# Optimization experiments

Hardware: AMD Instinct MI355X
Metric: run time of the kernel (lower is better)

Reference implementation:

```python
import jax, jax.numpy as jnp
import numpy as np

B, S, D, H = 2, 2048, 2048, 32
DH = D // H
NEG = -1e9


def setup_inputs() -> dict:
    key = jax.random.key(0)
    ks = jax.random.split(key, 10)
    sc = 0.02
    hidden_state = jax.random.normal(ks[0], (B, S, D), dtype=jnp.float32)
    # additive causal mask, broadcastable to [B,H,S,S]
    causal = jnp.tril(jnp.ones((S, S), dtype=bool))
    mask = jnp.where(causal, 0.0, NEG).astype(jnp.float32)[None, None]
    return {
        "hidden_state": hidden_state,
        "mask": mask,
        "q_w": jax.random.normal(ks[1], (D, D), jnp.float32) * sc,
        "q_b": jnp.zeros((D,), jnp.float32),
        "k_w": jax.random.normal(ks[2], (D, D), jnp.float32) * sc,
        "k_b": jnp.zeros((D,), jnp.float32),
        "v_w": jax.random.normal(ks[3], (D, D), jnp.float32) * sc,
        "v_b": jnp.zeros((D,), jnp.float32),
        "o_w": jax.random.normal(ks[4], (D, D), jnp.float32) * sc,
        "o_b": jnp.zeros((D,), jnp.float32),
    }


def reference(hidden_state, mask, q_w, q_b, k_w, k_b, v_w, v_b, o_w, o_b):
    scale = DH ** -0.5
    # projections (torch Linear: x @ W^T + b)
    q = (hidden_state @ q_w.T + q_b).reshape(B, S, H, DH).transpose(0, 2, 1, 3) * scale
    k = (hidden_state @ k_w.T + k_b).reshape(B, S, H, DH).transpose(0, 2, 1, 3)
    v = (hidden_state @ v_w.T + v_b).reshape(B, S, H, DH).transpose(0, 2, 1, 3)
    qk = jnp.einsum('bhqd,bhkd->bhqk', q, k) + mask
    attn = jax.nn.softmax(qk, axis=-1)
    o = jnp.einsum('bhqk,bhkd->bhqd', attn, v)
    o = o.transpose(0, 2, 1, 3).reshape(B, S, D)
    return o @ o_w.T + o_b
```

## Files before the change

### kernel.cpp

```cpp
#include <hip/hip_runtime.h>
#include <stdint.h>

#define Hh   32
#define Ss   2048
#define Dd   2048
#define DHd  64
#define Mtok 4096
#define MiB  (1u << 20)
#define NTK  32

typedef unsigned short u16;
typedef u16   u16x4  __attribute__((ext_vector_type(4)));
typedef u16   u16x8  __attribute__((ext_vector_type(8)));
typedef short bf16x8 __attribute__((ext_vector_type(8)));
typedef float f32x4  __attribute__((ext_vector_type(4)));

__device__ __forceinline__ u16 f2bf(float f) {
    union { float f; uint32_t u; } v; v.f = f;
    uint32_t r = v.u + 0x7fffu + ((v.u >> 16) & 1u);
    return (u16)(r >> 16);
}
__device__ __forceinline__ uint32_t cvtpk_bf16(float lo, float hi) {
    uint32_t r;
    asm volatile("v_cvt_pk_bf16_f32 %0, %1, %2" : "=v"(r) : "v"(lo), "v"(hi));
    return r;
}
__device__ __forceinline__ void gld_lds16(const void* g, void* l) {
    __builtin_amdgcn_global_load_lds(
        (const __attribute__((address_space(1))) uint32_t*)g,
        (__attribute__((address_space(3))) uint32_t*)l,
        16, 0, 0);
}
#define SB() __builtin_amdgcn_sched_barrier(0)

__global__ void cvt_all(const float* __restrict__ x,  const float* __restrict__ qw,
                        const float* __restrict__ kw, const float* __restrict__ vw,
                        const float* __restrict__ ow,
                        u16* __restrict__ Xb, u16* __restrict__ Wcat, u16* __restrict__ Wob)
{
    const size_t nX = 1u << 23, nW = 1u << 22;
    size_t i = ((size_t)blockIdx.x * 256 + threadIdx.x) * 8;
    const float* src; u16* dst; size_t off;
    if (i < nX) { src = x; dst = Xb; off = i; }
    else {
        size_t j = i - nX;
        int seg = (int)(j >> 22);
        off = j & (nW - 1);
        src = (seg == 0) ? qw : (seg == 1) ? kw : (seg == 2) ? vw : ow;
        dst = (seg == 3) ? Wob : Wcat + (size_t)seg * nW;
    }
    f32x4 a = *(const f32x4*)(src + off);
    f32x4 b = *(const f32x4*)(src + off + 4);
    u16x8 o;
    o[0] = f2bf(a[0]); o[1] = f2bf(a[1]); o[2] = f2bf(a[2]); o[3] = f2bf(a[3]);
    o[4] = f2bf(b[0]); o[5] = f2bf(b[1]); o[6] = f2bf(b[2]); o[7] = f2bf(b[3]);
    *(u16x8*)(dst + off) = o;
}


__device__ __forceinline__ void stage_unitA(const u16* __restrict__ src, u16* dst, int wid, int lane)
{
    const int P = wid * 64 + lane;
    const int rp = P >> 3, c4p = P & 7, c4 = c4p ^ (rp & 7);
    const int r = rp * 2 + (c4 >> 2), c = (c4 & 3) * 8;
    gld_lds16(src + (size_t)r * Dd + c, dst + wid * 512);
}
__device__ __forceinline__ void stage_unitB(const u16* __restrict__ src, u16* dst, int wid, int lane)
{
#pragma unroll
    for (int j = 0; j < 2; ++j) {
        const int P = j * 512 + wid * 64 + lane;
        const int rp = P >> 3, c4p = P & 7, c4 = c4p ^ (rp & 7);
        const int r = rp * 2 + (c4 >> 2), c = (c4 & 3) * 8;
        gld_lds16(src + (size_t)r * Dd + c, dst + j * 4096 + wid * 512);
    }
}
__device__ __forceinline__ bf16x8 frag_read(const u16* unit, int r, int lg)
{
    const int rp = r >> 1;
    const int c4 = ((r & 1) << 2) | lg;
    const int c4p = c4 ^ (rp & 7);
    return *(const bf16x8*)(unit + rp * 64 + c4p * 8);
}

__device__ __forceinline__ void gemm2_core(const u16* __restrict__ Ab, const u16* __restrict__ Wb,
                                           u16* L, f32x4 acc[4][4],
                                           int wid, int lane, int l15, int lg, int wm, int wn)
{
    u16* const L0 = L;
    u16* const L1 = L + 24576;
    stage_unitA(Ab + 0,  L0 + 0,     wid, lane);
    stage_unitB(Wb + 0,  L0 + 8192,  wid, lane);
    stage_unitA(Ab + 32, L0 + 4096,  wid, lane);
    stage_unitB(Wb + 32, L0 + 16384, wid, lane);
    stage_unitA(Ab + 64, L1 + 0,     wid, lane);
    stage_unitB(Wb + 64, L1 + 8192,  wid, lane);
    asm volatile("s_waitcnt vmcnt(6)" ::: "memory");
    SB(); __builtin_amdgcn_s_barrier(); SB();

    const int aro = wm * 64 + l15;
    const int bro = wn * 64 + l15;
#pragma unroll 2
    for (int t = 0; t < NTK; ++t) {
        u16* const Lc = (t & 1) ? L1 : L0;
        u16* const Ln = (t & 1) ? L0 : L1;
#pragma unroll
        for (int ph = 0; ph < 2; ++ph) {
            const u16* Au = Lc + ph * 4096;
            const u16* Bu = Lc + 8192 + ph * 8192;
            bf16x8 bfr[4], a[4];
#pragma unroll
            for (int ni = 0; ni < 4; ++ni) bfr[ni] = frag_read(Bu, bro + ni * 16, lg);
#pragma unroll
            for (int mi = 0; mi < 4; ++mi) a[mi] = frag_read(Au, aro + mi * 16, lg);
            if (ph == 0) {
                if (t + 1 < NTK) {
                    stage_unitA(Ab + (t + 1) * 64 + 32, Ln + 4096,  wid, lane);
                    stage_unitB(Wb + (t + 1) * 64 + 32, Ln + 16384, wid, lane);
                }
            } else {
                if (t + 2 < NTK) {
                    stage_unitA(Ab + (t + 2) * 64, Lc + 0,    wid, lane);
                    stage_unitB(Wb + (t + 2) * 64, Lc + 8192, wid, lane);
                }
            }
            asm volatile("s_waitcnt lgkmcnt(0)" ::: "memory");
            SB();
            __builtin_amdgcn_s_setprio(1);
#pragma unroll
            for (int mi = 0; mi < 4; ++mi)
#pragma unroll
                for (int ni = 0; ni < 4; ++ni)
                    acc[mi][ni] = __builtin_amdgcn_mfma_f32_16x16x32_bf16(a[mi], bfr[ni], acc[mi][ni], 0, 0, 0);
            __builtin_amdgcn_s_setprio(0);
            const bool deep = (ph == 0) ? (t + 1 < NTK) : (t + 2 < NTK);
            if (deep) { asm volatile("s_waitcnt vmcnt(6)" ::: "memory"); }
            else      { asm volatile("s_waitcnt vmcnt(0)" ::: "memory"); }
            SB(); __builtin_amdgcn_s_barrier(); SB();
        }
    }
}

__global__ __launch_bounds__(512) void gemm_qkv8(
    const u16* __restrict__ X, const u16* __restrict__ Wcat,
    const float* __restrict__ Bq, const float* __restrict__ Bk, const float* __restrict__ Bv,
    u16* __restrict__ Qo, u16* __restrict__ Ko, u16* __restrict__ Vo)
{
    __shared__ __align__(16) u16 L[2 * 24576];
    const int tid = threadIdx.x, wid = tid >> 6, lane = tid & 63;
    const int l15 = lane & 15, lg = lane >> 4;
    const int wm = wid >> 2, wn = wid & 3;
    const int m0 = blockIdx.x * 128, n0 = blockIdx.y * 256;

    f32x4 acc[4][4] = {};
    gemm2_core(X + (size_t)m0 * Dd, Wcat + (size_t)n0 * Dd, L, acc, wid, lane, l15, lg, wm, wn);

#pragma unroll
    for (int ni = 0; ni < 4; ++ni) {
        const int n = n0 + wn * 64 + ni * 16 + l15;
        const int z = n >> 11, nn = n & 2047;
        const float bv = (z == 0 ? Bq : z == 1 ? Bk : Bv)[nn];
        const float sc = (z == 0) ? 0.125f : 1.0f;
        u16* Out = (z == 0 ? Qo : z == 1 ? Ko : Vo);
        const int h = nn >> 6, dh = nn & 63;
#pragma unroll
        for (int mi = 0; mi < 4; ++mi)
#pragma unroll
            for (int r = 0; r < 4; ++r) {
                const int m = m0 + wm * 64 + mi * 16 + lg * 4 + r;
                const int b = m >> 11, s = m & 2047;
                Out[(((size_t)b * Hh + h) * Ss + s) * DHd + dh] = f2bf((acc[mi][ni][r] + bv) * sc);
            }
    }
}

__global__ __launch_bounds__(512) void gemm_oproj8(
    const u16* __restrict__ A, const u16* __restrict__ W,
    const float* __restrict__ Bi, float* __restrict__ Out)
{
    __shared__ __align__(16) u16 L[2 * 24576];
    const int tid = threadIdx.x, wid = tid >> 6, lane = tid & 63;
    const int l15 = lane & 15, lg = lane >> 4;
    const int wm = wid >> 2, wn = wid & 3;
    const int m0 = blockIdx.x * 128, n0 = blockIdx.y * 256;

    f32x4 acc[4][4] = {};
    gemm2_core(A + (size_t)m0 * Dd, W + (size_t)n0 * Dd, L, acc, wid, lane, l15, lg, wm, wn);

#pragma unroll
    for (int ni = 0; ni < 4; ++ni) {
        const int n = n0 + wn * 64 + ni * 16 + l15;
        const float bv = Bi[n];
#pragma unroll
        for (int mi = 0; mi < 4; ++mi)
#pragma unroll
            for (int r = 0; r < 4; ++r) {
                const int m = m0 + wm * 64 + mi * 16 + lg * 4 + r;
                Out[(size_t)m * Dd + n] = acc[mi][ni][r] + bv;
            }
    }
}

__global__ void transpose_v(const u16* __restrict__ Vsrc, u16* __restrict__ Vdst)
{
    __shared__ __align__(16) u16 t[64 * 68];
    const int bh = blockIdx.y, s0 = blockIdx.x * 64;
    const int tid = threadIdx.x;
    {
        const int r = tid >> 2, cq = (tid & 3) * 16;
        const u16* src = Vsrc + ((size_t)bh * Ss + s0 + r) * DHd;
#pragma unroll
        for (int j = 0; j < 4; ++j) {
            u16x4 v = *(const u16x4*)(src + cq + j * 4);
            *(u16x4*)&t[r * 68 + cq + j * 4] = v;
        }
    }
    __syncthreads();
    {
        const int d = tid >> 2, sq = (tid & 3) * 16;
        u16* dst = Vdst + ((size_t)bh * DHd + d) * Ss + s0;
#pragma unroll
        for (int j = 0; j < 4; ++j) {
            u16x4 v;
            v.x = t[(sq + j * 4 + 0) * 68 + d];
            v.y = t[(sq + j * 4 + 1) * 68 + d];
            v.z = t[(sq + j * 4 + 2) * 68 + d];
            v.w = t[(sq + j * 4 + 3) * 68 + d];
            *(u16x4*)(dst + sq + j * 4) = v;
        }
    }
}

__device__ __forceinline__ void stage_kv(const u16* __restrict__ Kg, const u16* __restrict__ Vg,
                                         u16* Kl, u16* Vl, int kv0, int tid)
{
    const int u    = tid;
    const int row  = u >> 3;
    const int csrc = ((u & 7) ^ (row & 7)) * 8;
    const int base = (u & ~63) * 8;
    gld_lds16(Kg + (size_t)(kv0 + row) * DHd + csrc, Kl + base);
    gld_lds16(Vg + (size_t)row * Ss + kv0 + csrc, Vl + base);
}

__device__ __forceinline__ void attn_tile(
    const u16* __restrict__ Kc, const u16* __restrict__ Vc, int kv0,
    int q0, int qrow, int l15, int lg, int psw,
    const bf16x8* __restrict__ bq, f32x4* __restrict__ o,
    float& m_r, float& l_r, char* __restrict__ prow)
{
    if (kv0 > q0 + 15) return;
    f32x4 s[4] = {};
    __builtin_amdgcn_s_setprio(1);
#pragma unroll
    for (int nb = 0; nb < 4; ++nb) {
        const int krow = nb * 16 + l15;
        const char* rb = (const char*)(Kc + krow * 64);
        const int sw = (krow & 7) << 4;
#pragma unroll
        for (int kf = 0; kf < 2; ++kf) {
            bf16x8 ak = *(const bf16x8*)(rb + ((kf * 64 + lg * 16) ^ sw));
            s[nb] = __builtin_amdgcn_mfma_f32_16x16x32_bf16(ak, bq[kf], s[nb], 0, 0, 0);
        }
    }
    __builtin_amdgcn_s_setprio(0);
    if (kv0 + 63 > q0) {
#pragma unroll
        for (int nb = 0; nb < 4; ++nb)
#pragma unroll
            for (int r = 0; r < 4; ++r)
                if (kv0 + nb * 16 + lg * 4 + r > qrow) s[nb][r] = -3e38f;
    }
    float pm = -3e38f;
#pragma unroll
    for (int nb = 0; nb < 4; ++nb)
#pragma unroll
        for (int r = 0; r < 4; ++r) pm = fmaxf(pm, s[nb][r]);
    pm = fmaxf(pm, __shfl_xor(pm, 16, 64));
    pm = fmaxf(pm, __shfl_xor(pm, 32, 64));
    const bool full = !__all(pm - m_r <= 8.0f);
    float mn = m_r, al = 1.0f;
    if (full) {
        mn = fmaxf(m_r, pm);
        al = __expf(m_r - mn);
#pragma unroll
        for (int nb = 0; nb < 4; ++nb)
#pragma unroll
            for (int r = 0; r < 4; ++r) o[nb][r] *= al;
    }
    float rs = 0.f;
    float p[4][4];
#pragma unroll
    for (int nb = 0; nb < 4; ++nb)
#pragma unroll
        for (int r = 0; r < 4; ++r) { p[nb][r] = __expf(s[nb][r] - mn); rs += p[nb][r]; }
    rs += __shfl_xor(rs, 16, 64);
    rs += __shfl_xor(rs, 32, 64);
    l_r = l_r * al + rs;
    m_r = mn;
#pragma unroll
    for (int nb = 0; nb < 4; ++nb) {
        const uint32_t w0 = cvtpk_bf16(p[nb][0], p[nb][1]);
        const uint32_t w1 = cvtpk_bf16(p[nb][2], p[nb][3]);
        const int c0 = (nb * 32 + lg * 8) ^ psw;
        *(uint32_t*)(prow + c0)     = w0;
        *(uint32_t*)(prow + c0 + 4) = w1;
    }
    bf16x8 pa[2];
#pragma unroll
    for (int ks = 0; ks < 2; ++ks)
        pa[ks] = *(const bf16x8*)(prow + ((ks * 64 + lg * 16) ^ psw));
    __builtin_amdgcn_s_setprio(1);
#pragma unroll
    for (int nb = 0; nb < 4; ++nb) {
        const int vrow = nb * 16 + l15;
        const char* rb = (const char*)(Vc + vrow * 64);
        const int sw = (vrow & 7) << 4;
#pragma unroll
        for (int ks = 0; ks < 2; ++ks) {
            bf16x8 bv = *(const bf16x8*)(rb + ((ks * 64 + lg * 16) ^ sw));
            o[nb] = __builtin_amdgcn_mfma_f32_16x16x32_bf16(bv, pa[ks], o[nb], 0, 0, 0);
        }
    }
    __builtin_amdgcn_s_setprio(0);
}

__global__ __launch_bounds__(512) void attn(
    const u16* __restrict__ Qb, const u16* __restrict__ Kb,
    const u16* __restrict__ Vt, u16* __restrict__ Ob)
{
    __shared__ __align__(16) u16 Kl[2][4096];
    __shared__ __align__(16) u16 Vl[2][4096];
    __shared__ __align__(16) u16 PlA[8][1024];
    __shared__ __align__(16) u16 PlB[8][1024];
    const int bh = blockIdx.y;
    const int b = bh >> 5, h = bh & 31;
    const int tid = threadIdx.x;
    const int wid = tid >> 6, lane = tid & 63;
    const int l15 = lane & 15, lg = lane >> 4;
    const int bxA = blockIdx.x, bxB = 15 - bxA;
    const int q0A = bxA * 128 + wid * 16, q0B = bxB * 128 + wid * 16;
    const int qrowA = q0A + l15, qrowB = q0B + l15;
    char* prowA = (char*)PlA[wid] + l15 * 128;
    char* prowB = (char*)PlB[wid] + l15 * 128;
    const int psw = (l15 & 7) << 4;

    const u16* Kp = Kb + (size_t)bh * Ss * DHd;
    const u16* Vp = Vt + (size_t)bh * DHd * Ss;

    bf16x8 bqA[2], bqB[2];
    {
        const u16* QpA = Qb + ((size_t)bh * Ss + q0A) * DHd;
        const u16* QpB = Qb + ((size_t)bh * Ss + q0B) * DHd;
#pragma unroll
        for (int kf = 0; kf < 2; ++kf) {
            bqA[kf] = *(const bf16x8*)(QpA + (size_t)l15 * DHd + kf * 32 + lg * 8);
            bqB[kf] = *(const bf16x8*)(QpB + (size_t)l15 * DHd + kf * 32 + lg * 8);
        }
    }
    asm volatile("s_waitcnt vmcnt(0)" ::: "memory");

    f32x4 oA[4] = {}, oB[4] = {};
    float mA = -3e38f, lA = 0.f, mB = -3e38f, lB = 0.f;
    const int nt = 2 * (bxB + 1);

    stage_kv(Kp, Vp, Kl[0], Vl[0], 0, tid);
    for (int t = 0; t < nt; ++t) {
        if (t + 1 < nt) {
            stage_kv(Kp, Vp, Kl[(t + 1) & 1], Vl[(t + 1) & 1], (t + 1) * 64, tid);
            asm volatile("s_waitcnt vmcnt(2)" ::: "memory");
        } else {
            asm volatile("s_waitcnt vmcnt(0)" ::: "memory");
        }
        SB(); __builtin_amdgcn_s_barrier(); SB();
        const int kv0 = t * 64;
        attn_tile(Kl[t & 1], Vl[t & 1], kv0, q0A, qrowA, l15, lg, psw, bqA, oA, mA, lA, prowA);
        attn_tile(Kl[t & 1], Vl[t & 1], kv0, q0B, qrowB, l15, lg, psw, bqB, oB, mB, lB, prowB);
        SB(); __builtin_amdgcn_s_barrier(); SB();
    }

    {
        const float inv = 1.0f / lA;
        u16* orow = Ob + ((size_t)b * Ss + qrowA) * Dd + h * DHd;
#pragma unroll
        for (int nb = 0; nb < 4; ++nb) {
            u16x4 pk;
#pragma unroll
            for (int r = 0; r < 4; ++r) pk[r] = f2bf(oA[nb][r] * inv);
            *(u16x4*)(orow + nb * 16 + lg * 4) = pk;
        }
    }
    {
        const float inv = 1.0f / lB;
        u16* orow = Ob + ((size_t)b * Ss + qrowB) * Dd + h * DHd;
#pragma unroll
        for (int nb = 0; nb < 4; ++nb) {
            u16x4 pk;
#pragma unroll
            for (int r = 0; r < 4; ++r) pk[r] = f2bf(oB[nb][r] * inv);
            *(u16x4*)(orow + nb * 16 + lg * 4) = pk;
        }
    }
}

extern "C" void kernel_launch(void* const* d_in, const int* in_sizes, int n_in,
                              void* d_out, int out_size, void* d_ws, size_t ws_size,
                              hipStream_t stream)
{
    (void)in_sizes; (void)n_in; (void)out_size; (void)ws_size;
    const float* x  = (const float*)d_in[0];
    const float* qw = (const float*)d_in[2];
    const float* qb = (const float*)d_in[3];
    const float* kw = (const float*)d_in[4];
    const float* kb = (const float*)d_in[5];
    const float* vw = (const float*)d_in[6];
    const float* vb = (const float*)d_in[7];
    const float* ow = (const float*)d_in[8];
    const float* obias = (const float*)d_in[9];

    uint8_t* ws = (uint8_t*)d_ws;
    u16* Xb  = (u16*)(ws);
    u16* Wcat= (u16*)(ws + 16 * MiB);
    u16* Wob = (u16*)(ws + 40 * MiB);
    u16* Qb  = (u16*)(ws + 48 * MiB);
    u16* Kb  = (u16*)(ws + 64 * MiB);
    u16* Vb  = (u16*)(ws + 80 * MiB);
    u16* Vt  = Xb;
    u16* Ob  = Vb;

    cvt_all<<<12288, 256, 0, stream>>>(x, qw, kw, vw, ow, Xb, Wcat, Wob);

    gemm_qkv8<<<dim3(Mtok / 128, 6144 / 256), dim3(512), 0, stream>>>(
        Xb, Wcat, qb, kb, vb, Qb, Kb, Vb);
    transpose_v<<<dim3(Ss / 64, 64), dim3(256), 0, stream>>>(Vb, Vt);
    attn<<<dim3(8, 64), dim3(512), 0, stream>>>(Qb, Kb, Vt, Ob);
    gemm_oproj8<<<dim3(Mtok / 128, Dd / 256), dim3(512), 0, stream>>>(
        Ob, Wob, obias, (float*)d_out);
}
```

Before: 239.2 us.

## Load GEMM A fragments directly from global, shrink LDS, swizzle block order

The GEMM core no longer stages the activation (A) tile through LDS. Each wave reads its A fragments straight from global memory into registers, and only the weight tile is staged, which cuts LDS use per block and adds a launch-bounds occupancy hint. Blocks are remapped with an XCD-style swizzle on a 1D grid so that neighbouring blocks share tiles in cache. The risk is that direct global loads of A repeat across the four wn waves and lose the latency hiding that the prefetch pipeline gave, since the A loads are issued in the same phase they are consumed.

```diff
diff --git a/kernel.cpp b/kernel.cpp
--- a/kernel.cpp
+++ b/kernel.cpp
@@ -58,13 +58,6 @@
 }
 
 
-__device__ __forceinline__ void stage_unitA(const u16* __restrict__ src, u16* dst, int wid, int lane)
-{
-    const int P = wid * 64 + lane;
-    const int rp = P >> 3, c4p = P & 7, c4 = c4p ^ (rp & 7);
-    const int r = rp * 2 + (c4 >> 2), c = (c4 & 3) * 8;
-    gld_lds16(src + (size_t)r * Dd + c, dst + wid * 512);
-}
 __device__ __forceinline__ void stage_unitB(const u16* __restrict__ src, u16* dst, int wid, int lane)
 {
 #pragma unroll
@@ -88,42 +81,39 @@
                                            int wid, int lane, int l15, int lg, int wm, int wn)
 {
     u16* const L0 = L;
-    u16* const L1 = L + 24576;
-    stage_unitA(Ab + 0,  L0 + 0,     wid, lane);
-    stage_unitB(Wb + 0,  L0 + 8192,  wid, lane);
-    stage_unitA(Ab + 32, L0 + 4096,  wid, lane);
-    stage_unitB(Wb + 32, L0 + 16384, wid, lane);
-    stage_unitA(Ab + 64, L1 + 0,     wid, lane);
-    stage_unitB(Wb + 64, L1 + 8192,  wid, lane);
-    asm volatile("s_waitcnt vmcnt(6)" ::: "memory");
+    u16* const L1 = L + 16384;
+    stage_unitB(Wb + 0,  L0 + 0,    wid, lane);
+    stage_unitB(Wb + 32, L0 + 8192, wid, lane);
+    stage_unitB(Wb + 64, L1 + 0,    wid, lane);
+    asm volatile("s_waitcnt vmcnt(4)" ::: "memory");
     SB(); __builtin_amdgcn_s_barrier(); SB();
 
-    const int aro = wm * 64 + l15;
-    const int bro = wn * 64 + l15;
+    const int arow = wm * 64 + l15;
+    const int bro  = wn * 64 + l15;
 #pragma unroll 2
     for (int t = 0; t < NTK; ++t) {
         u16* const Lc = (t & 1) ? L1 : L0;
         u16* const Ln = (t & 1) ? L0 : L1;
 #pragma unroll
         for (int ph = 0; ph < 2; ++ph) {
-            const u16* Au = Lc + ph * 4096;
-            const u16* Bu = Lc + 8192 + ph * 8192;
+            const u16* Bu = Lc + ph * 8192;
             bf16x8 bfr[4], a[4];
 #pragma unroll
             for (int ni = 0; ni < 4; ++ni) bfr[ni] = frag_read(Bu, bro + ni * 16, lg);
-#pragma unroll
-            for (int mi = 0; mi < 4; ++mi) a[mi] = frag_read(Au, aro + mi * 16, lg);
+            const int kc = t * 64 + ph * 32 + lg * 8;
+#pragma unroll
+            for (int mi = 0; mi < 4; ++mi)
+                a[mi] = *(const bf16x8*)(Ab + (size_t)(arow + mi * 16) * Dd + kc);
+            bool staged;
             if (ph == 0) {
-                if (t + 1 < NTK) {
-                    stage_unitA(Ab + (t + 1) * 64 + 32, Ln + 4096,  wid, lane);
-                    stage_unitB(Wb + (t + 1) * 64 + 32, Ln + 16384, wid, lane);
-                }
+                staged = (t + 1 < NTK);
+                if (staged) stage_unitB(Wb + (t + 1) * 64 + 32, Ln + 8192, wid, lane);
             } else {
-                if (t + 2 < NTK) {
-                    stage_unitA(Ab + (t + 2) * 64, Lc + 0,    wid, lane);
-                    stage_unitB(Wb + (t + 2) * 64, Lc + 8192, wid, lane);
-                }
+                staged = (t + 2 < NTK);
+                if (staged) stage_unitB(Wb + (t + 2) * 64, Lc + 0, wid, lane);
             }
+            if (staged) { asm volatile("s_waitcnt vmcnt(2)" ::: "memory"); }
+            else        { asm volatile("s_waitcnt vmcnt(0)" ::: "memory"); }
             asm volatile("s_waitcnt lgkmcnt(0)" ::: "memory");
             SB();
             __builtin_amdgcn_s_setprio(1);
@@ -133,24 +123,23 @@
                 for (int ni = 0; ni < 4; ++ni)
                     acc[mi][ni] = __builtin_amdgcn_mfma_f32_16x16x32_bf16(a[mi], bfr[ni], acc[mi][ni], 0, 0, 0);
             __builtin_amdgcn_s_setprio(0);
-            const bool deep = (ph == 0) ? (t + 1 < NTK) : (t + 2 < NTK);
-            if (deep) { asm volatile("s_waitcnt vmcnt(6)" ::: "memory"); }
-            else      { asm volatile("s_waitcnt vmcnt(0)" ::: "memory"); }
             SB(); __builtin_amdgcn_s_barrier(); SB();
         }
     }
 }
 
-__global__ __launch_bounds__(512) void gemm_qkv8(
+__global__ __launch_bounds__(512, 4) void gemm_qkv8(
     const u16* __restrict__ X, const u16* __restrict__ Wcat,
     const float* __restrict__ Bq, const float* __restrict__ Bk, const float* __restrict__ Bv,
     u16* __restrict__ Qo, u16* __restrict__ Ko, u16* __restrict__ Vo)
 {
-    __shared__ __align__(16) u16 L[2 * 24576];
+    __shared__ __align__(16) u16 L[2 * 16384];
     const int tid = threadIdx.x, wid = tid >> 6, lane = tid & 63;
     const int l15 = lane & 15, lg = lane >> 4;
     const int wm = wid >> 2, wn = wid & 3;
-    const int m0 = blockIdx.x * 128, n0 = blockIdx.y * 256;
+    const int bid = blockIdx.x;
+    const int swz = (bid & 7) * 96 + (bid >> 3);
+    const int m0 = (swz / 24) * 128, n0 = (swz % 24) * 256;
 
     f32x4 acc[4][4] = {};
     gemm2_core(X + (size_t)m0 * Dd, Wcat + (size_t)n0 * Dd, L, acc, wid, lane, l15, lg, wm, wn);
@@ -174,15 +163,17 @@
     }
 }
 
-__global__ __launch_bounds__(512) void gemm_oproj8(
+__global__ __launch_bounds__(512, 4) void gemm_oproj8(
     const u16* __restrict__ A, const u16* __restrict__ W,
     const float* __restrict__ Bi, float* __restrict__ Out)
 {
-    __shared__ __align__(16) u16 L[2 * 24576];
+    __shared__ __align__(16) u16 L[2 * 16384];
     const int tid = threadIdx.x, wid = tid >> 6, lane = tid & 63;
     const int l15 = lane & 15, lg = lane >> 4;
     const int wm = wid >> 2, wn = wid & 3;
-    const int m0 = blockIdx.x * 128, n0 = blockIdx.y * 256;
+    const int bid = blockIdx.x;
+    const int swz = (bid & 7) * 32 + (bid >> 3);
+    const int m0 = (swz >> 3) * 128, n0 = (swz & 7) * 256;
 
     f32x4 acc[4][4] = {};
     gemm2_core(A + (size_t)m0 * Dd, W + (size_t)n0 * Dd, L, acc, wid, lane, l15, lg, wm, wn);
@@ -429,10 +420,8 @@
 
     cvt_all<<<12288, 256, 0, stream>>>(x, qw, kw, vw, ow, Xb, Wcat, Wob);
 
-    gemm_qkv8<<<dim3(Mtok / 128, 6144 / 256), dim3(512), 0, stream>>>(
-        Xb, Wcat, qb, kb, vb, Qb, Kb, Vb);
+    gemm_qkv8<<<768, 512, 0, stream>>>(Xb, Wcat, qb, kb, vb, Qb, Kb, Vb);
     transpose_v<<<dim3(Ss / 64, 64), dim3(256), 0, stream>>>(Vb, Vt);
     attn<<<dim3(8, 64), dim3(512), 0, stream>>>(Qb, Kb, Vt, Ob);
-    gemm_oproj8<<<dim3(Mtok / 128, Dd / 256), dim3(512), 0, stream>>>(
-        Ob, Wob, obias, (float*)d_out);
-}
+    gemm_oproj8<<<256, 512, 0, stream>>>(Ob, Wob, obias, (float*)d_out);
+}
```

Result: slower. 572.6 us (+139.4%).

## Enlarge QKV GEMM tile to 256x256 with swizzled block order

Applied to the files above, without the earlier changes.

Replaces the 128x256 QKV projection GEMM with a 256x256 tile kernel that gives each wave 8x4 accumulator fragments. It uses a new double-buffered LDS pipeline that splits the MFMA work into low and high halves to overlap LDS reads. Block indices are remapped with a grouping swizzle to improve L2 reuse of A/W panels. The larger tile raises arithmetic intensity but doubles accumulator registers and LDS use, and halves the grid to 384 blocks, which may hurt occupancy and load balance.

```diff
diff --git a/kernel.cpp b/kernel.cpp
--- a/kernel.cpp
+++ b/kernel.cpp
@@ -56,7 +56,6 @@
     o[4] = f2bf(b[0]); o[5] = f2bf(b[1]); o[6] = f2bf(b[2]); o[7] = f2bf(b[3]);
     *(u16x8*)(dst + off) = o;
 }
-
 
 __device__ __forceinline__ void stage_unitA(const u16* __restrict__ src, u16* dst, int wid, int lane)
 {
@@ -141,19 +140,92 @@
     }
 }
 
-__global__ __launch_bounds__(512) void gemm_qkv8(
+__device__ __forceinline__ void gemm256_core(const u16* __restrict__ Ab, const u16* __restrict__ Wb,
+                                             u16* L, f32x4 acc[8][4],
+                                             int wid, int lane, int l15, int lg, int wm, int wn)
+{
+    u16* const L0 = L;
+    u16* const L1 = L + 32768;
+    stage_unitB(Ab + 0,  L0 + 0,     wid, lane);
+    stage_unitB(Wb + 0,  L0 + 16384, wid, lane);
+    stage_unitB(Ab + 32, L0 + 8192,  wid, lane);
+    stage_unitB(Wb + 32, L0 + 24576, wid, lane);
+    stage_unitB(Ab + 64, L1 + 0,     wid, lane);
+    stage_unitB(Wb + 64, L1 + 16384, wid, lane);
+    asm volatile("s_waitcnt vmcnt(4)" ::: "memory");
+    SB(); __builtin_amdgcn_s_barrier(); SB();
+
+    const int arow = wm * 128 + l15;
+    const int bro  = wn * 64 + l15;
+#pragma unroll 2
+    for (int t = 0; t < NTK; ++t) {
+        u16* const Lc = (t & 1) ? L1 : L0;
+        u16* const Ln = (t & 1) ? L0 : L1;
+#pragma unroll
+        for (int sp = 0; sp < 2; ++sp) {
+            const u16* Au = Lc + sp * 8192;
+            const u16* Bu = Lc + 16384 + sp * 8192;
+            bf16x8 bfr[4], alo[4], ahi[4];
+#pragma unroll
+            for (int ni = 0; ni < 4; ++ni) bfr[ni] = frag_read(Bu, bro + ni * 16, lg);
+#pragma unroll
+            for (int mi = 0; mi < 4; ++mi) alo[mi] = frag_read(Au, arow + mi * 16, lg);
+#pragma unroll
+            for (int mi = 0; mi < 4; ++mi) ahi[mi] = frag_read(Au, arow + (mi + 4) * 16, lg);
+            bool staged;
+            if (sp == 0) {
+                staged = (t + 1 < NTK);
+                if (staged) {
+                    stage_unitB(Ab + (t + 1) * 64 + 32, Ln + 8192,  wid, lane);
+                    stage_unitB(Wb + (t + 1) * 64 + 32, Ln + 24576, wid, lane);
+                }
+            } else {
+                staged = (t + 2 < NTK);
+                if (staged) {
+                    stage_unitB(Ab + (t + 2) * 64, Lc + 0,     wid, lane);
+                    stage_unitB(Wb + (t + 2) * 64, Lc + 16384, wid, lane);
+                }
+            }
+            asm volatile("s_waitcnt lgkmcnt(4)" ::: "memory");
+            SB();
+            __builtin_amdgcn_s_setprio(1);
+#pragma unroll
+            for (int mi = 0; mi < 4; ++mi)
+#pragma unroll
+                for (int ni = 0; ni < 4; ++ni)
+                    acc[mi][ni] = __builtin_amdgcn_mfma_f32_16x16x32_bf16(alo[mi], bfr[ni], acc[mi][ni], 0, 0, 0);
+            __builtin_amdgcn_s_setprio(0);
+            asm volatile("s_waitcnt lgkmcnt(0)" ::: "memory");
+            SB();
+            __builtin_amdgcn_s_setprio(1);
+#pragma unroll
+            for (int mi = 0; mi < 4; ++mi)
+#pragma unroll
+                for (int ni = 0; ni < 4; ++ni)
+                    acc[mi + 4][ni] = __builtin_amdgcn_mfma_f32_16x16x32_bf16(ahi[mi], bfr[ni], acc[mi + 4][ni], 0, 0, 0);
+            __builtin_amdgcn_s_setprio(0);
+            if (staged) { asm volatile("s_waitcnt vmcnt(4)" ::: "memory"); }
+            else        { asm volatile("s_waitcnt vmcnt(0)" ::: "memory"); }
+            SB(); __builtin_amdgcn_s_barrier(); SB();
+        }
+    }
+}
+
+__global__ __launch_bounds__(512, 2) void gemm_qkv256(
     const u16* __restrict__ X, const u16* __restrict__ Wcat,
     const float* __restrict__ Bq, const float* __restrict__ Bk, const float* __restrict__ Bv,
     u16* __restrict__ Qo, u16* __restrict__ Ko, u16* __restrict__ Vo)
 {
-    __shared__ __align__(16) u16 L[2 * 24576];
+    __shared__ __align__(16) u16 L[2 * 32768];
     const int tid = threadIdx.x, wid = tid >> 6, lane = tid & 63;
     const int l15 = lane & 15, lg = lane >> 4;
     const int wm = wid >> 2, wn = wid & 3;
-    const int m0 = blockIdx.x * 128, n0 = blockIdx.y * 256;
-
-    f32x4 acc[4][4] = {};
-    gemm2_core(X + (size_t)m0 * Dd, Wcat + (size_t)n0 * Dd, L, acc, wid, lane, l15, lg, wm, wn);
+    const int bid = blockIdx.x;
+    const int swz = (bid & 7) * 48 + (bid >> 3);
+    const int m0 = (swz / 24) * 256, n0 = (swz % 24) * 256;
+
+    f32x4 acc[8][4] = {};
+    gemm256_core(X + (size_t)m0 * Dd, Wcat + (size_t)n0 * Dd, L, acc, wid, lane, l15, lg, wm, wn);
 
 #pragma unroll
     for (int ni = 0; ni < 4; ++ni) {
@@ -164,10 +236,10 @@
         u16* Out = (z == 0 ? Qo : z == 1 ? Ko : Vo);
         const int h = nn >> 6, dh = nn & 63;
 #pragma unroll
-        for (int mi = 0; mi < 4; ++mi)
+        for (int mi = 0; mi < 8; ++mi)
 #pragma unroll
             for (int r = 0; r < 4; ++r) {
-                const int m = m0 + wm * 64 + mi * 16 + lg * 4 + r;
+                const int m = m0 + wm * 128 + mi * 16 + lg * 4 + r;
                 const int b = m >> 11, s = m & 2047;
                 Out[(((size_t)b * Hh + h) * Ss + s) * DHd + dh] = f2bf((acc[mi][ni][r] + bv) * sc);
             }
@@ -429,8 +501,7 @@
 
     cvt_all<<<12288, 256, 0, stream>>>(x, qw, kw, vw, ow, Xb, Wcat, Wob);
 
-    gemm_qkv8<<<dim3(Mtok / 128, 6144 / 256), dim3(512), 0, stream>>>(
-        Xb, Wcat, qb, kb, vb, Qb, Kb, Vb);
+    gemm_qkv256<<<384, 512, 0, stream>>>(Xb, Wcat, qb, kb, vb, Qb, Kb, Vb);
     transpose_v<<<dim3(Ss / 64, 64), dim3(256), 0, stream>>>(Vb, Vt);
     attn<<<dim3(8, 64), dim3(512), 0, stream>>>(Qb, Kb, Vt, Ob);
     gemm_oproj8<<<dim3(Mtok / 128, Dd / 256), dim3(512), 0, stream>>>(
```

Measured after the change: 258.0 us. +7.9%, slower.
